# Kernel optimization log

Hardware: AMD Instinct MI355X
Metric: run time of the kernel (lower is better)

## Reference

```python
import jax, jax.numpy as jnp
import numpy as np

NUM_SAMPLED = 8192
NUM_CLASSES = 50000
DIM = 512
BATCH = 8192


def _log_uniform_expected(ids, num_sampled, num_classes):
    # log-uniform sampler probability: P(c) = (log(c+2) - log(c+1)) / log(V+1)
    c = ids.astype(jnp.float32)
    p = (jnp.log(c + 2.0) - jnp.log(c + 1.0)) / jnp.log(float(num_classes + 1))
    # expected count under unique sampling of num_sampled candidates (as in TF)
    return -jnp.expm1(float(num_sampled) * jnp.log1p(-p))


def setup_inputs() -> dict:
    key = jax.random.key(0)
    k1, k2, k3, k4, k5 = jax.random.split(key, 5)
    inputs = jax.random.normal(k1, (BATCH, DIM), jnp.float32)
    labels = jax.random.randint(k2, (BATCH, 1), 0, NUM_CLASSES)
    kernel = jax.random.uniform(k3, (NUM_CLASSES, DIM), jnp.float32, -0.05, 0.05)
    bias = jax.random.uniform(k4, (NUM_CLASSES,), jnp.float32, -0.05, 0.05)
    sampled = jax.random.randint(k5, (NUM_SAMPLED,), 0, NUM_CLASSES)
    return {"inputs": inputs, "labels": labels, "kernel": kernel,
            "bias": bias, "sampled": sampled}


def reference(inputs, labels, kernel, bias, sampled):
    # tf.nn.sampled_softmax_loss (train branch), num_true=1,
    # log-uniform sampler, remove_accidental_hits=True.
    labels_flat = labels[:, 0]

    # true logits: gather one weight row per example, dot with input
    w_true = kernel[labels_flat]                      # [B, D]
    b_true = bias[labels_flat]                        # [B]
    true_logits = jnp.einsum('bd,bd->b', inputs, w_true) + b_true
    true_logits = true_logits - jnp.log(
        _log_uniform_expected(labels_flat, NUM_SAMPLED, NUM_CLASSES))

    # sampled logits: gather S candidate rows, small matmul [B,D]x[D,S]
    w_samp = kernel[sampled]                          # [S, D]
    b_samp = bias[sampled]                            # [S]
    sampled_logits = jnp.einsum('bd,sd->bs', inputs, w_samp) + b_samp[None, :]
    sampled_logits = sampled_logits - jnp.log(
        _log_uniform_expected(sampled, NUM_SAMPLED, NUM_CLASSES))

    # remove accidental hits: mask sampled candidates that equal the true label
    hits = labels_flat[:, None] == sampled[None, :]   # [B, S]
    sampled_logits = jnp.where(hits, -1e9, sampled_logits)

    # softmax CE with the true class at column 0
    logits = jnp.concatenate([true_logits[:, None], sampled_logits], axis=1)
    loss = jax.nn.logsumexp(logits, axis=1) - logits[:, 0]  # [B]
    return loss
```

## Files before the change

kernel.cpp:

```cpp
#include <hip/hip_runtime.h>
#include <hip/hip_bf16.h>
#include <cstdint>
#include <cstddef>

#define BATCH   8192
#define NSAMP   8192
#define DIM     512
#define NCLASS  50000

typedef __attribute__((ext_vector_type(8))) short bf16x8;
typedef __attribute__((ext_vector_type(4))) float f32x4;

__device__ __forceinline__ float neg_log_expected(int c) {
    double p = log1p(1.0 / (double)(c + 1)) / log((double)(NCLASS + 1));
    double e = -expm1((double)NSAMP * log1p(-p));
    return (float)(-log(e));
}

__device__ __forceinline__ unsigned short f2bf(float f) {
    __hip_bfloat16 h = __float2bfloat16(f);
    return *reinterpret_cast<unsigned short*>(&h);
}

__device__ __forceinline__ void gload_lds16(const void* g, void* l) {
    __builtin_amdgcn_global_load_lds(
        (const __attribute__((address_space(1))) void*)g,
        (__attribute__((address_space(3))) void*)l, 16, 0, 0);
}

__global__ void k_fused(const float* __restrict__ inputs, const int* __restrict__ labels,
                        const float* __restrict__ W, const float* __restrict__ bias,
                        __hip_bfloat16* __restrict__ Abf,
                        float* __restrict__ true_logit, float* __restrict__ row_sum) {
    int row = blockIdx.x;
    int t   = threadIdx.x;
    float4 v = reinterpret_cast<const float4*>(inputs + (size_t)row * DIM)[t];
    ushort4 u;
    u.x = f2bf(v.x); u.y = f2bf(v.y); u.z = f2bf(v.z); u.w = f2bf(v.w);
    reinterpret_cast<ushort4*>(Abf + (size_t)row * DIM)[t] = u;

    int lbl = labels[row];
    float4 w = reinterpret_cast<const float4*>(W + (size_t)lbl * DIM)[t];
    float dot = v.x * w.x + v.y * w.y + v.z * w.z + v.w * w.w;
    #pragma unroll
    for (int off = 32; off; off >>= 1) dot += __shfl_down(dot, off, 64);
    __shared__ float red[2];
    if ((t & 63) == 0) red[t >> 6] = dot;
    __syncthreads();
    if (t == 0) {
        float tl = red[0] + red[1] + bias[lbl] + neg_log_expected(lbl);
        true_logit[row] = tl;
        row_sum[row]    = __expf(tl);
    }
}

__global__ void k_gather(const float* __restrict__ W, const float* __restrict__ bias,
                         const int* __restrict__ sampled,
                         __hip_bfloat16* __restrict__ Bbf, float* __restrict__ adj) {
    int s   = blockIdx.x;
    int idx = sampled[s];
    float4 v = reinterpret_cast<const float4*>(W + (size_t)idx * DIM)[threadIdx.x];
    ushort4 u;
    u.x = f2bf(v.x); u.y = f2bf(v.y); u.z = f2bf(v.z); u.w = f2bf(v.w);
    reinterpret_cast<ushort4*>(Bbf + (size_t)s * DIM)[threadIdx.x] = u;
    if (threadIdx.x == 0) adj[s] = bias[idx] + neg_log_expected(idx);
}

__global__ __launch_bounds__(512, 6) void k_gemm(
    const __hip_bfloat16* __restrict__ A, const __hip_bfloat16* __restrict__ B,
    const float* __restrict__ adj, const int* __restrict__ labels,
    const int* __restrict__ sampled, float* __restrict__ row_sum) {
    __shared__ alignas(16) __hip_bfloat16 Asm[2][128 * 32];
    __shared__ alignas(16) __hip_bfloat16 Bsm[2][128 * 32];
    __shared__ float tsum[2][128];

    const int tid  = threadIdx.x;
    const int wave = tid >> 6;
    const int lane = tid & 63;
    const int wm   = wave >> 1;
    const int wn   = wave & 1;

    const int bid  = blockIdx.x;
    const int xcd  = bid & 7;
    const int u    = bid >> 3;
    const int rb   = xcd * 8 + (u & 7);
    const int cgrp = u >> 3;
    const int brow = rb * 128;

    const int srow = lane >> 2;
    const int sg   = (lane & 3) ^ ((lane >> 3) & 3);
    const int rsel = lane & 15;
    const int koff = ((lane >> 4) ^ ((lane >> 1) & 3)) * 8;

    f32x4 acc[2][4];
    #pragma unroll
    for (int m = 0; m < 2; ++m)
        #pragma unroll
        for (int n = 0; n < 4; ++n)
            acc[m][n] = (f32x4){0.f, 0.f, 0.f, 0.f};

    const __hip_bfloat16* pa = A + (size_t)(brow + wave * 16 + srow) * DIM + sg * 8;
    const __hip_bfloat16* pb = B + (size_t)(cgrp * 512 + wave * 16 + srow) * DIM + sg * 8;

    auto stage = [&](int buf) {
        gload_lds16(pa, &Asm[buf][(wave * 16) * 32]);
        gload_lds16(pb, &Bsm[buf][(wave * 16) * 32]);
    };
    auto advance = [&](int snext) {
        const bool tb = (snext & 15) == 0;
        const ptrdiff_t dA = tb ? (ptrdiff_t)-480 : (ptrdiff_t)32;
        const ptrdiff_t dB = tb ? (ptrdiff_t)(128 * DIM - 480) : (ptrdiff_t)32;
        pa += dA; pb += dB;
    };

    auto body = [&](int buf) {
        bf16x8 a[2], b[4];
        #pragma unroll
        for (int m = 0; m < 2; ++m)
            a[m] = *reinterpret_cast<const bf16x8*>(
                &Asm[buf][(wm * 32 + m * 16 + rsel) * 32 + koff]);
        #pragma unroll
        for (int n = 0; n < 4; ++n)
            b[n] = *reinterpret_cast<const bf16x8*>(
                &Bsm[buf][(wn * 64 + n * 16 + rsel) * 32 + koff]);
        #pragma unroll
        for (int m = 0; m < 2; ++m)
            #pragma unroll
            for (int n = 0; n < 4; ++n)
                acc[m][n] = __builtin_amdgcn_mfma_f32_16x16x32_bf16(a[m], b[n], acc[m][n], 0, 0, 0);
    };

    auto epi = [&](int t) {
        const int bcol = (cgrp * 4 + t) * 128;
        int sv[4]; float aadj[4];
        #pragma unroll
        for (int n = 0; n < 4; ++n) {
            int col = bcol + wn * 64 + n * 16 + rsel;
            aadj[n] = adj[col];
            sv[n]   = sampled[col];
        }
        #pragma unroll
        for (int m = 0; m < 2; ++m) {
            #pragma unroll
            for (int r = 0; r < 4; ++r) {
                int lr  = wm * 32 + m * 16 + (lane >> 4) * 4 + r;
                int lbl = labels[brow + lr];
                float part = 0.f;
                #pragma unroll
                for (int n = 0; n < 4; ++n) {
                    float logit = acc[m][n][r] + aadj[n];
                    part += (sv[n] == lbl) ? 0.f : __expf(logit);
                }
                part += __shfl_xor(part, 1, 16);
                part += __shfl_xor(part, 2, 16);
                part += __shfl_xor(part, 4, 16);
                part += __shfl_xor(part, 8, 16);
                if (rsel == 0) tsum[wn][lr] = part;
            }
        }
        __syncthreads();
        if (tid < 128)
            atomicAdd(&row_sum[brow + tid], tsum[0][tid] + tsum[1][tid]);
        #pragma unroll
        for (int m = 0; m < 2; ++m)
            #pragma unroll
            for (int n = 0; n < 4; ++n)
                acc[m][n] = (f32x4){0.f, 0.f, 0.f, 0.f};
    };

    stage(0);
    advance(1);
    __syncthreads();

    #pragma unroll 1
    for (int g = 0; g < 64; ++g) {
        if (g < 63) { stage((g + 1) & 1); advance(g + 2); }
        body(g & 1);
        if ((g & 15) == 15) epi(g >> 4);
        __syncthreads();
    }
}

__global__ void k_final(const float* __restrict__ row_sum,
                        const float* __restrict__ true_logit,
                        float* __restrict__ loss) {
    int i = blockIdx.x * blockDim.x + threadIdx.x;
    loss[i] = logf(row_sum[i]) - true_logit[i];
}

extern "C" void kernel_launch(void* const* d_in, const int* in_sizes, int n_in,
                              void* d_out, int out_size, void* d_ws, size_t ws_size,
                              hipStream_t stream) {
    const float* inputs  = (const float*)d_in[0];
    const int*   labels  = (const int*)d_in[1];
    const float* W       = (const float*)d_in[2];
    const float* bias    = (const float*)d_in[3];
    const int*   sampled = (const int*)d_in[4];
    float*       loss    = (float*)d_out;

    char* ws = (char*)d_ws;
    __hip_bfloat16* Abf = (__hip_bfloat16*)ws;
    __hip_bfloat16* Bbf = (__hip_bfloat16*)(ws + (size_t)BATCH * DIM * 2);
    float* adj        = (float*)(ws + (size_t)(BATCH + NSAMP) * DIM * 2);
    float* true_logit = adj + NSAMP;
    float* row_sum    = true_logit + BATCH;

    hipLaunchKernelGGL(k_fused, dim3(BATCH), dim3(128), 0, stream,
                       inputs, labels, W, bias, Abf, true_logit, row_sum);
    hipLaunchKernelGGL(k_gather, dim3(NSAMP), dim3(128), 0, stream,
                       W, bias, sampled, Bbf, adj);
    hipLaunchKernelGGL(k_gemm, dim3(1024), dim3(512), 0, stream,
                       Abf, Bbf, adj, labels, sampled, row_sum);
    hipLaunchKernelGGL(k_final, dim3(BATCH / 256), dim3(256), 0, stream,
                       row_sum, true_logit, loss);
}
```

Baseline: 136.8 us.

## Triple-buffer GEMM LDS pipeline with explicit waitcnt and merge prep kernels

The GEMM main loop moves from double to triple buffering of the LDS tiles. It keeps two global-to-LDS stages in flight and replaces __syncthreads with an explicit s_waitcnt vmcnt(2) plus s_barrier, so loads for later stages overlap the MFMA work. The last iteration is peeled to drain the pipeline. Separately, the input-conversion and sampled-row gather kernels are merged into one launch to save a kernel launch and its tail. The cost is more LDS per block, which may reduce occupancy, and hand-written waitcnt that relies on the ordering of global memory ops inside the epilogue.

```diff
diff --git a/kernel.cpp b/kernel.cpp
--- a/kernel.cpp
+++ b/kernel.cpp
@@ -28,50 +28,56 @@
         (__attribute__((address_space(3))) void*)l, 16, 0, 0);
 }
 
-__global__ void k_fused(const float* __restrict__ inputs, const int* __restrict__ labels,
-                        const float* __restrict__ W, const float* __restrict__ bias,
-                        __hip_bfloat16* __restrict__ Abf,
-                        float* __restrict__ true_logit, float* __restrict__ row_sum) {
-    int row = blockIdx.x;
+__global__ void k_prep(const float* __restrict__ inputs, const int* __restrict__ labels,
+                       const float* __restrict__ W, const float* __restrict__ bias,
+                       const int* __restrict__ sampled,
+                       __hip_bfloat16* __restrict__ Abf, __hip_bfloat16* __restrict__ Bbf,
+                       float* __restrict__ adj,
+                       float* __restrict__ true_logit, float* __restrict__ row_sum) {
+    int bid = blockIdx.x;
     int t   = threadIdx.x;
-    float4 v = reinterpret_cast<const float4*>(inputs + (size_t)row * DIM)[t];
-    ushort4 u;
-    u.x = f2bf(v.x); u.y = f2bf(v.y); u.z = f2bf(v.z); u.w = f2bf(v.w);
-    reinterpret_cast<ushort4*>(Abf + (size_t)row * DIM)[t] = u;
-
-    int lbl = labels[row];
-    float4 w = reinterpret_cast<const float4*>(W + (size_t)lbl * DIM)[t];
-    float dot = v.x * w.x + v.y * w.y + v.z * w.z + v.w * w.w;
-    #pragma unroll
-    for (int off = 32; off; off >>= 1) dot += __shfl_down(dot, off, 64);
-    __shared__ float red[2];
-    if ((t & 63) == 0) red[t >> 6] = dot;
-    __syncthreads();
-    if (t == 0) {
-        float tl = red[0] + red[1] + bias[lbl] + neg_log_expected(lbl);
-        true_logit[row] = tl;
-        row_sum[row]    = __expf(tl);
+    if (bid < BATCH) {
+        int row = bid;
+        float4 v = reinterpret_cast<const float4*>(inputs + (size_t)row * DIM)[t];
+        ushort4 u;
+        u.x = f2bf(v.x); u.y = f2bf(v.y); u.z = f2bf(v.z); u.w = f2bf(v.w);
+        reinterpret_cast<ushort4*>(Abf + (size_t)row * DIM)[t] = u;
+
+        int lbl = labels[row];
+        float4 w = reinterpret_cast<const float4*>(W + (size_t)lbl * DIM)[t];
+        float dot = v.x * w.x + v.y * w.y + v.z * w.z + v.w * w.w;
+        #pragma unroll
+        for (int off = 32; off; off >>= 1) dot += __shfl_down(dot, off, 64);
+        __shared__ float red[2];
+        if ((t & 63) == 0) red[t >> 6] = dot;
+        __syncthreads();
+        if (t == 0) {
+            float tl = red[0] + red[1] + bias[lbl] + neg_log_expected(lbl);
+            true_logit[row] = tl;
+            row_sum[row]    = __expf(tl);
+        }
+    } else {
+        int s   = bid - BATCH;
+        int idx = sampled[s];
+        float4 v = reinterpret_cast<const float4*>(W + (size_t)idx * DIM)[t];
+        ushort4 u;
+        u.x = f2bf(v.x); u.y = f2bf(v.y); u.z = f2bf(v.z); u.w = f2bf(v.w);
+        reinterpret_cast<ushort4*>(Bbf + (size_t)s * DIM)[t] = u;
+        if (t == 0) adj[s] = bias[idx] + neg_log_expected(idx);
     }
 }
 
-__global__ void k_gather(const float* __restrict__ W, const float* __restrict__ bias,
-                         const int* __restrict__ sampled,
-                         __hip_bfloat16* __restrict__ Bbf, float* __restrict__ adj) {
-    int s   = blockIdx.x;
-    int idx = sampled[s];
-    float4 v = reinterpret_cast<const float4*>(W + (size_t)idx * DIM)[threadIdx.x];
-    ushort4 u;
-    u.x = f2bf(v.x); u.y = f2bf(v.y); u.z = f2bf(v.z); u.w = f2bf(v.w);
-    reinterpret_cast<ushort4*>(Bbf + (size_t)s * DIM)[threadIdx.x] = u;
-    if (threadIdx.x == 0) adj[s] = bias[idx] + neg_log_expected(idx);
-}
+
+#define BARRIER()  asm volatile("s_barrier" ::: "memory")
+#define LBARRIER() asm volatile("s_waitcnt lgkmcnt(0)\n\ts_barrier" ::: "memory")
+#define VMCNT(n)   asm volatile("s_waitcnt vmcnt(" #n ")" ::: "memory")
 
 __global__ __launch_bounds__(512, 6) void k_gemm(
     const __hip_bfloat16* __restrict__ A, const __hip_bfloat16* __restrict__ B,
     const float* __restrict__ adj, const int* __restrict__ labels,
     const int* __restrict__ sampled, float* __restrict__ row_sum) {
-    __shared__ alignas(16) __hip_bfloat16 Asm[2][128 * 32];
-    __shared__ alignas(16) __hip_bfloat16 Bsm[2][128 * 32];
+    __shared__ alignas(16) __hip_bfloat16 Asm[3][128 * 32];
+    __shared__ alignas(16) __hip_bfloat16 Bsm[3][128 * 32];
     __shared__ float tsum[2][128];
 
     const int tid  = threadIdx.x;
@@ -158,7 +164,7 @@
                 if (rsel == 0) tsum[wn][lr] = part;
             }
         }
-        __syncthreads();
+        LBARRIER();
         if (tid < 128)
             atomicAdd(&row_sum[brow + tid], tsum[0][tid] + tsum[1][tid]);
         #pragma unroll
@@ -168,17 +174,22 @@
                 acc[m][n] = (f32x4){0.f, 0.f, 0.f, 0.f};
     };
 
-    stage(0);
-    advance(1);
-    __syncthreads();
+    stage(0); advance(1);
+    stage(1); advance(2);
 
     #pragma unroll 1
-    for (int g = 0; g < 64; ++g) {
-        if (g < 63) { stage((g + 1) & 1); advance(g + 2); }
-        body(g & 1);
+    for (int g = 0; g < 63; ++g) {
+        VMCNT(2);
+        BARRIER();
+        const int cur = g % 3;
+        if (g < 62) { stage((g + 2) % 3); advance(g + 3); }
+        body(cur);
         if ((g & 15) == 15) epi(g >> 4);
-        __syncthreads();
     }
+    VMCNT(0);
+    BARRIER();
+    body(0);
+    epi(3);
 }
 
 __global__ void k_final(const float* __restrict__ row_sum,
@@ -205,10 +216,9 @@
     float* true_logit = adj + NSAMP;
     float* row_sum    = true_logit + BATCH;
 
-    hipLaunchKernelGGL(k_fused, dim3(BATCH), dim3(128), 0, stream,
-                       inputs, labels, W, bias, Abf, true_logit, row_sum);
-    hipLaunchKernelGGL(k_gather, dim3(NSAMP), dim3(128), 0, stream,
-                       W, bias, sampled, Bbf, adj);
+    hipLaunchKernelGGL(k_prep, dim3(BATCH + NSAMP), dim3(128), 0, stream,
+                       inputs, labels, W, bias, sampled, Abf, Bbf, adj,
+                       true_logit, row_sum);
     hipLaunchKernelGGL(k_gemm, dim3(1024), dim3(512), 0, stream,
                        Abf, Bbf, adj, labels, sampled, row_sum);
     hipLaunchKernelGGL(k_final, dim3(BATCH / 256), dim3(256), 0, stream,
```

New measurement: 130.4 us. 4.7% less time.
